# Kernel optimization log

Hardware: AMD Instinct MI355X
Metric: run time of the kernel (lower is better)

The kernel has to match this reference:

```python
import jax, jax.numpy as jnp
import numpy as np

B, C, H, W_ = 64, 768, 24, 24
POOL = 4  # pool_size
HID = 768


def setup_inputs() -> dict:
    key = jax.random.key(0)
    ks = jax.random.split(key, 12)
    search_feat = jax.random.normal(ks[0], (B, C, H, W_), dtype=jnp.float32)
    # valid normalized boxes (x0,y0,x1,y1) in [0,1]
    cx = jax.random.uniform(ks[1], (B,), minval=0.25, maxval=0.75)
    cy = jax.random.uniform(ks[2], (B,), minval=0.25, maxval=0.75)
    bw = jax.random.uniform(ks[3], (B,), minval=0.1, maxval=0.5)
    bh = jax.random.uniform(ks[4], (B,), minval=0.1, maxval=0.5)
    x0 = jnp.clip(cx - bw / 2, 0.0, 1.0)
    x1 = jnp.clip(cx + bw / 2, 0.0, 1.0)
    y0 = jnp.clip(cy - bh / 2, 0.0, 1.0)
    y1 = jnp.clip(cy + bh / 2, 0.0, 1.0)
    search_box = jnp.stack([x0, y0, x1, y1], axis=1).astype(jnp.float32)
    sc = 0.02
    w1 = jax.random.normal(ks[5], (C, HID), dtype=jnp.float32) * sc
    b1 = jnp.zeros((HID,), jnp.float32)
    w2 = jax.random.normal(ks[6], (HID, HID), dtype=jnp.float32) * sc
    b2 = jnp.zeros((HID,), jnp.float32)
    w3 = jax.random.normal(ks[7], (HID, 1), dtype=jnp.float32) * sc
    b3 = jnp.zeros((1,), jnp.float32)
    return dict(search_feat=search_feat, search_box=search_box,
                w1=w1, b1=b1, w2=w2, b2=b2, w3=w3, b3=b3)


def _hat_cdf(t):
    # CDF of the triangular (bilinear) kernel tri(u)=max(0,1-|u|):
    # F(t) = integral_{-inf}^{t} tri(u) du
    return jnp.where(t <= -1.0, 0.0,
           jnp.where(t <= 0.0, 0.5 * (t + 1.0) ** 2,
           jnpp := jnp.where(t <= 1.0, 1.0 - 0.5 * (1.0 - t) ** 2, 1.0)))


def _bin_weights(lo, hi, n):
    # lo, hi: [B, P] bin edges in continuous pixel coords.
    # Returns [B, P, n]: integral of hat centered at each integer pixel over [lo, hi].
    c = jnp.arange(n, dtype=lo.dtype)
    return _hat_cdf(hi[..., None] - c) - _hat_cdf(lo[..., None] - c)


def reference(search_feat, search_box, w1, b1, w2, b2, w3, b3):
    b, c, h, w = search_feat.shape
    box = search_box * w  # module scales normalized coords by feature width
    x0, y0, x1, y1 = box[:, 0], box[:, 1], box[:, 2], box[:, 3]
    bw = (x1 - x0) / POOL  # per-roi bin width
    bh = (y1 - y0) / POOL
    i = jnp.arange(POOL, dtype=box.dtype)
    ex_lo = x0[:, None] + i * bw[:, None]   # [B, P]
    ex_hi = ex_lo + bw[:, None]
    ey_lo = y0[:, None] + i * bh[:, None]
    ey_hi = ey_lo + bh[:, None]
    # PrRoIPool: exact integral of bilinearly-interpolated feature over each bin.
    # Bilinear interp is a separable hat-basis expansion (zero outside the map),
    # so the 2D integral factors into per-axis weights.
    Wx = _bin_weights(ex_lo, ex_hi, w)      # [B, P, W]
    Wy = _bin_weights(ey_lo, ey_hi, h)      # [B, P, H]
    raw = jnp.einsum('bph,bchw,bqw->bcpq', Wy, search_feat, Wx)
    area = (bw * bh)[:, None, None, None]
    pooled = jnp.where(area > 0, raw / jnp.maximum(area, 1e-12), 0.0)  # [B,C,P,P]
    # rearrange 'b c h w -> b (h w) c' then AdaptiveAvgPool1d(1) over tokens
    feat = jnp.mean(pooled, axis=(2, 3))[:, None, :]  # [B, 1, C]
    x = jax.nn.relu(feat @ w1 + b1)
    x = jax.nn.relu(x @ w2 + b2)
    out = x @ w3 + b3                                  # [B, 1, 1]
    return out
```

## Files before the change

### kernel.cpp

```cpp
#include <hip/hip_runtime.h>

#define B_DIM 64
#define C_DIM 768
#define HID_DIM 768
#define PLANE 576
#define PLANE4 144
#define KC 48
#define OT 64

__device__ __forceinline__ float hatcdf(float t) {
    float u = fminf(fmaxf(t, -1.f), 1.f);
    float a = u + 1.f;
    float b = 1.f - u;
    return (t <= 0.f) ? 0.5f * a * a : 1.f - 0.5f * b * b;
}

__global__ __launch_bounds__(256) void pool_kernel(
    const float* __restrict__ X, const float* __restrict__ box,
    float* __restrict__ feat, float* __restrict__ zbuf)
{
    const int t = threadIdx.x;
    const int bx = blockIdx.x;
    if (bx < 96) {
        reinterpret_cast<float4*>(zbuf)[bx * 256 + t] = make_float4(0.f, 0.f, 0.f, 0.f);
    }
    const int b = bx >> 5;

    __shared__ float wx[24], wy[24];
    __shared__ float sscale;
    if (t < 49) {
        const float x0 = box[b * 4 + 0] * 24.f;
        const float y0 = box[b * 4 + 1] * 24.f;
        const float x1 = box[b * 4 + 2] * 24.f;
        const float y1 = box[b * 4 + 3] * 24.f;
        if (t < 24) {
            wx[t] = hatcdf(x1 - (float)t) - hatcdf(x0 - (float)t);
        } else if (t < 48) {
            const int h = t - 24;
            wy[h] = hatcdf(y1 - (float)h) - hatcdf(y0 - (float)h);
        } else {
            const float bw = (x1 - x0) * 0.25f;
            const float bh = (y1 - y0) * 0.25f;
            const float area = bw * bh;
            sscale = (area > 0.f) ? 1.f / (16.f * fmaxf(area, 1e-12f)) : 0.f;
        }
    }
    __syncthreads();

    const int wave = t >> 6;
    const int lane = t & 63;
    const int c0 = (bx & 31) * 24 + wave * 6;
    const float4* __restrict__ P =
        reinterpret_cast<const float4*>(X + ((size_t)b * C_DIM + c0) * PLANE);

    float acc[6];
    #pragma unroll
    for (int r = 0; r < 6; ++r) acc[r] = 0.f;

    #pragma unroll
    for (int r = 0; r < 6; ++r) {
        const float4* __restrict__ Q = P + r * PLANE4;
        int f = lane;
        float4 v = Q[f];
        int h = f / 6, wb = (f - h * 6) * 4;
        acc[r] += wy[h] * (v.x * wx[wb] + v.y * wx[wb + 1] + v.z * wx[wb + 2] + v.w * wx[wb + 3]);
        f = lane + 64;
        v = Q[f];
        h = f / 6; wb = (f - h * 6) * 4;
        acc[r] += wy[h] * (v.x * wx[wb] + v.y * wx[wb + 1] + v.z * wx[wb + 2] + v.w * wx[wb + 3]);
        if (lane < 16) {
            f = lane + 128;
            v = Q[f];
            h = f / 6; wb = (f - h * 6) * 4;
            acc[r] += wy[h] * (v.x * wx[wb] + v.y * wx[wb + 1] + v.z * wx[wb + 2] + v.w * wx[wb + 3]);
        }
    }

    #pragma unroll
    for (int r = 0; r < 6; ++r) {
        float a = acc[r];
        #pragma unroll
        for (int off = 32; off; off >>= 1) a += __shfl_down(a, off);
        if (lane == 0) feat[(size_t)b * C_DIM + c0 + r] = a * sscale;
    }
}

template <bool RELU_IN>
__global__ __launch_bounds__(256) void fc_chunk(
    const float* __restrict__ A, const float* __restrict__ bias,
    const float* __restrict__ Wm, float* __restrict__ Out)
{
    __shared__ float As[KC][68];
    __shared__ float Ws[KC][68];
    const int t = threadIdx.x;
    const int ot = blockIdx.x * OT;
    const int kc = blockIdx.y * KC;

    #pragma unroll
    for (int j = t; j < B_DIM * (KC / 4); j += 256) {
        const int bb = j / (KC / 4);
        const int k4 = (j % (KC / 4)) * 4;
        float4 v = *reinterpret_cast<const float4*>(A + (size_t)bb * HID_DIM + kc + k4);
        if constexpr (RELU_IN) {
            const float4 bv = *reinterpret_cast<const float4*>(bias + kc + k4);
            v.x = fmaxf(v.x + bv.x, 0.f);
            v.y = fmaxf(v.y + bv.y, 0.f);
            v.z = fmaxf(v.z + bv.z, 0.f);
            v.w = fmaxf(v.w + bv.w, 0.f);
        }
        As[k4 + 0][bb] = v.x;
        As[k4 + 1][bb] = v.y;
        As[k4 + 2][bb] = v.z;
        As[k4 + 3][bb] = v.w;
    }
    #pragma unroll
    for (int j = t; j < KC * (OT / 4); j += 256) {
        const int k = j / (OT / 4);
        const int oo = (j % (OT / 4)) * 4;
        const float4 v = *reinterpret_cast<const float4*>(Wm + (size_t)(kc + k) * HID_DIM + ot + oo);
        *reinterpret_cast<float4*>(&Ws[k][oo]) = v;
    }
    __syncthreads();

    const int b0 = (t >> 4) * 4;
    const int o0 = (t & 15) * 4;
    float acc[4][4] = {};
    #pragma unroll 6
    for (int k = 0; k < KC; ++k) {
        const float4 a = *reinterpret_cast<const float4*>(&As[k][b0]);
        const float4 w = *reinterpret_cast<const float4*>(&Ws[k][o0]);
        acc[0][0] += a.x * w.x; acc[0][1] += a.x * w.y; acc[0][2] += a.x * w.z; acc[0][3] += a.x * w.w;
        acc[1][0] += a.y * w.x; acc[1][1] += a.y * w.y; acc[1][2] += a.y * w.z; acc[1][3] += a.y * w.w;
        acc[2][0] += a.z * w.x; acc[2][1] += a.z * w.y; acc[2][2] += a.z * w.z; acc[2][3] += a.z * w.w;
        acc[3][0] += a.w * w.x; acc[3][1] += a.w * w.y; acc[3][2] += a.w * w.z; acc[3][3] += a.w * w.w;
    }
    #pragma unroll
    for (int i = 0; i < 4; ++i)
        #pragma unroll
        for (int j = 0; j < 4; ++j)
            atomicAdd(&Out[(size_t)(b0 + i) * HID_DIM + ot + o0 + j], acc[i][j]);
}

__global__ __launch_bounds__(256) void head_kernel(
    const float* __restrict__ x2raw, const float* __restrict__ b2,
    const float* __restrict__ w3, const float* __restrict__ b3,
    float* __restrict__ out)
{
    const int b = blockIdx.x;
    const int t = threadIdx.x;
    float acc = 0.f;
    for (int o = t; o < HID_DIM; o += 256)
        acc += fmaxf(x2raw[(size_t)b * HID_DIM + o] + b2[o], 0.f) * w3[o];
    #pragma unroll
    for (int off = 32; off; off >>= 1) acc += __shfl_down(acc, off);
    __shared__ float r[4];
    if ((t & 63) == 0) r[t >> 6] = acc;
    __syncthreads();
    if (t == 0) out[b] = r[0] + r[1] + r[2] + r[3] + b3[0];
}

extern "C" void kernel_launch(void* const* d_in, const int* in_sizes, int n_in,
                              void* d_out, int out_size, void* d_ws, size_t ws_size,
                              hipStream_t stream) {
    const float* X   = (const float*)d_in[0];
    const float* box = (const float*)d_in[1];
    const float* w1  = (const float*)d_in[2];
    const float* b1  = (const float*)d_in[3];
    const float* w2  = (const float*)d_in[4];
    const float* b2  = (const float*)d_in[5];
    const float* w3  = (const float*)d_in[6];
    const float* b3  = (const float*)d_in[7];
    float* out = (float*)d_out;

    float* feat  = (float*)d_ws;
    float* x1raw = feat + B_DIM * HID_DIM;
    float* x2raw = x1raw + B_DIM * HID_DIM;

    pool_kernel<<<2048, 256, 0, stream>>>(X, box, feat, x1raw);
    fc_chunk<false><<<dim3(HID_DIM / OT, HID_DIM / KC), 256, 0, stream>>>(feat, b1, w1, x1raw);
    fc_chunk<true><<<dim3(HID_DIM / OT, HID_DIM / KC), 256, 0, stream>>>(x1raw, b1, w2, x2raw);
    head_kernel<<<B_DIM, 256, 0, stream>>>(x2raw, b2, w3, b3, out);
}
```

Baseline: 214.3 us.

## Fuse pooling, MLP layers and head into one cooperative kernel

Replaces the four separate launches (ROI pooling, two FC layers, head) with a single cooperative kernel of 1024 blocks. Phases are separated by grid-wide syncs, and shared memory is reused across phases. Each pooling wave now handles 12 channels instead of 6. The aim is to remove inter-kernel launch gaps and tail effects. The cost is grid-sync overhead, fewer resident blocks during the bandwidth-bound pooling phase, and a fallback to the old four-kernel path if the cooperative launch fails.

After: 773.8 us. +261.1%, slower.

```diff
diff --git a/kernel.cpp b/kernel.cpp
--- a/kernel.cpp
+++ b/kernel.cpp
@@ -1,4 +1,7 @@
 #include <hip/hip_runtime.h>
+#include <hip/hip_cooperative_groups.h>
+
+namespace cg = cooperative_groups;
 
 #define B_DIM 64
 #define C_DIM 768
@@ -7,6 +10,7 @@
 #define PLANE4 144
 #define KC 48
 #define OT 64
+#define NBLK 1024
 
 __device__ __forceinline__ float hatcdf(float t) {
     float u = fminf(fmaxf(t, -1.f), 1.f);
@@ -15,6 +19,176 @@
     return (t <= 0.f) ? 0.5f * a * a : 1.f - 0.5f * b * b;
 }
 
+template <bool RELU_IN>
+__device__ __forceinline__ void fc_phase(
+    const float* __restrict__ A, const float* __restrict__ bias,
+    const float* __restrict__ Wm, float* __restrict__ Out,
+    float* __restrict__ As , float* __restrict__ Ws ,
+    int t, int ot, int kc)
+{
+    #pragma unroll
+    for (int j = t; j < B_DIM * (KC / 4); j += 256) {
+        const int bb = j / (KC / 4);
+        const int k4 = (j % (KC / 4)) * 4;
+        float4 v = *reinterpret_cast<const float4*>(A + (size_t)bb * HID_DIM + kc + k4);
+        if constexpr (RELU_IN) {
+            const float4 bv = *reinterpret_cast<const float4*>(bias + kc + k4);
+            v.x = fmaxf(v.x + bv.x, 0.f);
+            v.y = fmaxf(v.y + bv.y, 0.f);
+            v.z = fmaxf(v.z + bv.z, 0.f);
+            v.w = fmaxf(v.w + bv.w, 0.f);
+        }
+        As[(k4 + 0) * 68 + bb] = v.x;
+        As[(k4 + 1) * 68 + bb] = v.y;
+        As[(k4 + 2) * 68 + bb] = v.z;
+        As[(k4 + 3) * 68 + bb] = v.w;
+    }
+    #pragma unroll
+    for (int j = t; j < KC * (OT / 4); j += 256) {
+        const int k = j / (OT / 4);
+        const int oo = (j % (OT / 4)) * 4;
+        const float4 v = *reinterpret_cast<const float4*>(Wm + (size_t)(kc + k) * HID_DIM + ot + oo);
+        *reinterpret_cast<float4*>(&Ws[k * 68 + oo]) = v;
+    }
+    __syncthreads();
+
+    const int b0 = (t >> 4) * 4;
+    const int o0 = (t & 15) * 4;
+    float acc[4][4] = {};
+    #pragma unroll 6
+    for (int k = 0; k < KC; ++k) {
+        const float4 a = *reinterpret_cast<const float4*>(&As[k * 68 + b0]);
+        const float4 w = *reinterpret_cast<const float4*>(&Ws[k * 68 + o0]);
+        acc[0][0] += a.x * w.x; acc[0][1] += a.x * w.y; acc[0][2] += a.x * w.z; acc[0][3] += a.x * w.w;
+        acc[1][0] += a.y * w.x; acc[1][1] += a.y * w.y; acc[1][2] += a.y * w.z; acc[1][3] += a.y * w.w;
+        acc[2][0] += a.z * w.x; acc[2][1] += a.z * w.y; acc[2][2] += a.z * w.z; acc[2][3] += a.z * w.w;
+        acc[3][0] += a.w * w.x; acc[3][1] += a.w * w.y; acc[3][2] += a.w * w.z; acc[3][3] += a.w * w.w;
+    }
+    #pragma unroll
+    for (int i = 0; i < 4; ++i)
+        #pragma unroll
+        for (int j = 0; j < 4; ++j)
+            atomicAdd(&Out[(size_t)(b0 + i) * HID_DIM + ot + o0 + j], acc[i][j]);
+}
+
+template <int NP>
+__device__ __forceinline__ void pool_strip(
+    const float* __restrict__ X, int b, int c0, int lane,
+    const float* __restrict__ wx, const float* __restrict__ wy,
+    float sscale, float* __restrict__ feat)
+{
+    const float4* __restrict__ P =
+        reinterpret_cast<const float4*>(X + ((size_t)b * C_DIM + c0) * PLANE);
+    float acc[NP];
+    #pragma unroll
+    for (int r = 0; r < NP; ++r) acc[r] = 0.f;
+    #pragma unroll
+    for (int r = 0; r < NP; ++r) {
+        const float4* __restrict__ Q = P + r * PLANE4;
+        int f = lane;
+        float4 v = Q[f];
+        int h = f / 6, wb = (f - h * 6) * 4;
+        acc[r] += wy[h] * (v.x * wx[wb] + v.y * wx[wb + 1] + v.z * wx[wb + 2] + v.w * wx[wb + 3]);
+        f = lane + 64;
+        v = Q[f];
+        h = f / 6; wb = (f - h * 6) * 4;
+        acc[r] += wy[h] * (v.x * wx[wb] + v.y * wx[wb + 1] + v.z * wx[wb + 2] + v.w * wx[wb + 3]);
+        if (lane < 16) {
+            f = lane + 128;
+            v = Q[f];
+            h = f / 6; wb = (f - h * 6) * 4;
+            acc[r] += wy[h] * (v.x * wx[wb] + v.y * wx[wb + 1] + v.z * wx[wb + 2] + v.w * wx[wb + 3]);
+        }
+    }
+    #pragma unroll
+    for (int r = 0; r < NP; ++r) {
+        float a = acc[r];
+        #pragma unroll
+        for (int off = 32; off; off >>= 1) a += __shfl_down(a, off);
+        if (lane == 0) feat[(size_t)b * C_DIM + c0 + r] = a * sscale;
+    }
+}
+
+__global__ __launch_bounds__(256, 4) void fused_kernel(
+    const float* __restrict__ X, const float* __restrict__ box,
+    const float* __restrict__ w1, const float* __restrict__ b1,
+    const float* __restrict__ w2, const float* __restrict__ b2,
+    const float* __restrict__ w3, const float* __restrict__ b3,
+    float* __restrict__ out, float* __restrict__ ws)
+{
+    __shared__ float lds[2 * KC * 68];
+    float* feat  = ws;
+    float* x1raw = feat + B_DIM * HID_DIM;
+    float* x2raw = x1raw + B_DIM * HID_DIM;
+
+    const int t = threadIdx.x;
+    const int bx = blockIdx.x;
+    cg::grid_group grid = cg::this_grid();
+
+    if (bx < 96) {
+        reinterpret_cast<float4*>(x1raw)[bx * 256 + t] = make_float4(0.f, 0.f, 0.f, 0.f);
+    }
+    {
+        const int b = bx >> 4;
+        float* wx = lds;
+        float* wy = lds + 24;
+        float* ss = lds + 48;
+        if (t < 49) {
+            const float x0 = box[b * 4 + 0] * 24.f;
+            const float y0 = box[b * 4 + 1] * 24.f;
+            const float x1 = box[b * 4 + 2] * 24.f;
+            const float y1 = box[b * 4 + 3] * 24.f;
+            if (t < 24) {
+                wx[t] = hatcdf(x1 - (float)t) - hatcdf(x0 - (float)t);
+            } else if (t < 48) {
+                const int h = t - 24;
+                wy[h] = hatcdf(y1 - (float)h) - hatcdf(y0 - (float)h);
+            } else {
+                const float bw = (x1 - x0) * 0.25f;
+                const float bh = (y1 - y0) * 0.25f;
+                const float area = bw * bh;
+                ss[0] = (area > 0.f) ? 1.f / (16.f * fmaxf(area, 1e-12f)) : 0.f;
+            }
+        }
+        __syncthreads();
+        const int wave = t >> 6;
+        const int lane = t & 63;
+        const int c0 = (bx & 15) * 48 + wave * 12;
+        pool_strip<12>(X, b, c0, lane, wx, wy, ss[0], feat);
+    }
+    __threadfence();
+    grid.sync();
+
+    if (bx < (HID_DIM / OT) * (HID_DIM / KC)) {
+        const int ot = (bx % (HID_DIM / OT)) * OT;
+        const int kc = (bx / (HID_DIM / OT)) * KC;
+        fc_phase<false>(feat, b1, w1, x1raw, lds, lds + KC * 68, t, ot, kc);
+    }
+    __threadfence();
+    grid.sync();
+
+    if (bx < (HID_DIM / OT) * (HID_DIM / KC)) {
+        const int ot = (bx % (HID_DIM / OT)) * OT;
+        const int kc = (bx / (HID_DIM / OT)) * KC;
+        fc_phase<true>(x1raw, b1, w2, x2raw, lds, lds + KC * 68, t, ot, kc);
+    }
+    __threadfence();
+    grid.sync();
+
+    if (bx < B_DIM) {
+        const int b = bx;
+        float acc = 0.f;
+        for (int o = t; o < HID_DIM; o += 256)
+            acc += fmaxf(x2raw[(size_t)b * HID_DIM + o] + b2[o], 0.f) * w3[o];
+        #pragma unroll
+        for (int off = 32; off; off >>= 1) acc += __shfl_down(acc, off);
+        float* r = lds;
+        if ((t & 63) == 0) r[t >> 6] = acc;
+        __syncthreads();
+        if (t == 0) out[b] = r[0] + r[1] + r[2] + r[3] + b3[0];
+    }
+}
+
 __global__ __launch_bounds__(256) void pool_kernel(
     const float* __restrict__ X, const float* __restrict__ box,
     float* __restrict__ feat, float* __restrict__ zbuf)
@@ -25,7 +199,6 @@
         reinterpret_cast<float4*>(zbuf)[bx * 256 + t] = make_float4(0.f, 0.f, 0.f, 0.f);
     }
     const int b = bx >> 5;
-
     __shared__ float wx[24], wy[24];
     __shared__ float sscale;
     if (t < 49) {
@@ -46,43 +219,10 @@
         }
     }
     __syncthreads();
-
     const int wave = t >> 6;
     const int lane = t & 63;
     const int c0 = (bx & 31) * 24 + wave * 6;
-    const float4* __restrict__ P =
-        reinterpret_cast<const float4*>(X + ((size_t)b * C_DIM + c0) * PLANE);
-
-    float acc[6];
-    #pragma unroll
-    for (int r = 0; r < 6; ++r) acc[r] = 0.f;
-
-    #pragma unroll
-    for (int r = 0; r < 6; ++r) {
-        const float4* __restrict__ Q = P + r * PLANE4;
-        int f = lane;
-        float4 v = Q[f];
-        int h = f / 6, wb = (f - h * 6) * 4;
-        acc[r] += wy[h] * (v.x * wx[wb] + v.y * wx[wb + 1] + v.z * wx[wb + 2] + v.w * wx[wb + 3]);
-        f = lane + 64;
-        v = Q[f];
-        h = f / 6; wb = (f - h * 6) * 4;
-        acc[r] += wy[h] * (v.x * wx[wb] + v.y * wx[wb + 1] + v.z * wx[wb + 2] + v.w * wx[wb + 3]);
-        if (lane < 16) {
-            f = lane + 128;
-            v = Q[f];
-            h = f / 6; wb = (f - h * 6) * 4;
-            acc[r] += wy[h] * (v.x * wx[wb] + v.y * wx[wb + 1] + v.z * wx[wb + 2] + v.w * wx[wb + 3]);
-        }
-    }
-
-    #pragma unroll
-    for (int r = 0; r < 6; ++r) {
-        float a = acc[r];
-        #pragma unroll
-        for (int off = 32; off; off >>= 1) a += __shfl_down(a, off);
-        if (lane == 0) feat[(size_t)b * C_DIM + c0 + r] = a * sscale;
-    }
+    pool_strip<6>(X, b, c0, lane, wx, wy, sscale, feat);
 }
 
 template <bool RELU_IN>
@@ -90,55 +230,10 @@
     const float* __restrict__ A, const float* __restrict__ bias,
     const float* __restrict__ Wm, float* __restrict__ Out)
 {
-    __shared__ float As[KC][68];
-    __shared__ float Ws[KC][68];
-    const int t = threadIdx.x;
-    const int ot = blockIdx.x * OT;
-    const int kc = blockIdx.y * KC;
-
-    #pragma unroll
-    for (int j = t; j < B_DIM * (KC / 4); j += 256) {
-        const int bb = j / (KC / 4);
-        const int k4 = (j % (KC / 4)) * 4;
-        float4 v = *reinterpret_cast<const float4*>(A + (size_t)bb * HID_DIM + kc + k4);
-        if constexpr (RELU_IN) {
-            const float4 bv = *reinterpret_cast<const float4*>(bias + kc + k4);
-            v.x = fmaxf(v.x + bv.x, 0.f);
-            v.y = fmaxf(v.y + bv.y, 0.f);
-            v.z = fmaxf(v.z + bv.z, 0.f);
-            v.w = fmaxf(v.w + bv.w, 0.f);
-        }
-        As[k4 + 0][bb] = v.x;
-        As[k4 + 1][bb] = v.y;
-        As[k4 + 2][bb] = v.z;
-        As[k4 + 3][bb] = v.w;
-    }
-    #pragma unroll
-    for (int j = t; j < KC * (OT / 4); j += 256) {
-        const int k = j / (OT / 4);
-        const int oo = (j % (OT / 4)) * 4;
-        const float4 v = *reinterpret_cast<const float4*>(Wm + (size_t)(kc + k) * HID_DIM + ot + oo);
-        *reinterpret_cast<float4*>(&Ws[k][oo]) = v;
-    }
-    __syncthreads();
-
-    const int b0 = (t >> 4) * 4;
-    const int o0 = (t & 15) * 4;
-    float acc[4][4] = {};
-    #pragma unroll 6
-    for (int k = 0; k < KC; ++k) {
-        const float4 a = *reinterpret_cast<const float4*>(&As[k][b0]);
-        const float4 w = *reinterpret_cast<const float4*>(&Ws[k][o0]);
-        acc[0][0] += a.x * w.x; acc[0][1] += a.x * w.y; acc[0][2] += a.x * w.z; acc[0][3] += a.x * w.w;
-        acc[1][0] += a.y * w.x; acc[1][1] += a.y * w.y; acc[1][2] += a.y * w.z; acc[1][3] += a.y * w.w;
-        acc[2][0] += a.z * w.x; acc[2][1] += a.z * w.y; acc[2][2] += a.z * w.z; acc[2][3] += a.z * w.w;
-        acc[3][0] += a.w * w.x; acc[3][1] += a.w * w.y; acc[3][2] += a.w * w.z; acc[3][3] += a.w * w.w;
-    }
-    #pragma unroll
-    for (int i = 0; i < 4; ++i)
-        #pragma unroll
-        for (int j = 0; j < 4; ++j)
-            atomicAdd(&Out[(size_t)(b0 + i) * HID_DIM + ot + o0 + j], acc[i][j]);
+    __shared__ float As[KC * 68];
+    __shared__ float Ws[KC * 68];
+    fc_phase<RELU_IN>(A, bias, Wm, Out, As, Ws, threadIdx.x,
+                      blockIdx.x * OT, blockIdx.y * KC);
 }
 
 __global__ __launch_bounds__(256) void head_kernel(
@@ -171,13 +266,21 @@
     const float* w3  = (const float*)d_in[6];
     const float* b3  = (const float*)d_in[7];
     float* out = (float*)d_out;
-
-    float* feat  = (float*)d_ws;
-    float* x1raw = feat + B_DIM * HID_DIM;
-    float* x2raw = x1raw + B_DIM * HID_DIM;
-
-    pool_kernel<<<2048, 256, 0, stream>>>(X, box, feat, x1raw);
-    fc_chunk<false><<<dim3(HID_DIM / OT, HID_DIM / KC), 256, 0, stream>>>(feat, b1, w1, x1raw);
-    fc_chunk<true><<<dim3(HID_DIM / OT, HID_DIM / KC), 256, 0, stream>>>(x1raw, b1, w2, x2raw);
-    head_kernel<<<B_DIM, 256, 0, stream>>>(x2raw, b2, w3, b3, out);
-}
+    float* ws  = (float*)d_ws;
+
+    void* args[] = {(void*)&X, (void*)&box, (void*)&w1, (void*)&b1,
+                    (void*)&w2, (void*)&b2, (void*)&w3, (void*)&b3,
+                    (void*)&out, (void*)&ws};
+    hipError_t err = hipLaunchCooperativeKernel(
+        (const void*)fused_kernel, dim3(NBLK), dim3(256), args, 0, stream);
+
+    if (err != hipSuccess) {
+        float* feat  = ws;
+        float* x1raw = feat + B_DIM * HID_DIM;
+        float* x2raw = x1raw + B_DIM * HID_DIM;
+        pool_kernel<<<2048, 256, 0, stream>>>(X, box, feat, x1raw);
+        fc_chunk<false><<<dim3(HID_DIM / OT, HID_DIM / KC), 256, 0, stream>>>(feat, b1, w1, x1raw);
+        fc_chunk<true><<<dim3(HID_DIM / OT, HID_DIM / KC), 256, 0, stream>>>(x1raw, b1, w2, x2raw);
+        head_kernel<<<B_DIM, 256, 0, stream>>>(x2raw, b2, w3, b3, out);
+    }
+}
```
